# Kernel optimization log

Measured on AMD Instinct MI355X. Metric: run time of the kernel, lower is better.

## Reference

```python
import jax, jax.numpy as jnp
import numpy as np

EMBED_DIM = 256
NUM_HEADS = 8
TEMPERATURE = 10000.0
SCALE = 100.0
EPS = 1e-5


def setup_inputs() -> dict:
    key = jax.random.key(0)
    k1, k2, k3 = jax.random.split(key, 3)
    B, N, H, Wd = 1, 300, 24, 80
    # depths in a realistic positive range
    predict_depth = jax.random.uniform(k1, (B, N), dtype=jnp.float32) * 60.0
    depth_map = jax.random.uniform(k2, (B, H, Wd), dtype=jnp.float32) * 60.0
    # nn.Linear(embed_dim, num_heads): store as (in, out)
    W = jax.random.normal(k3, (EMBED_DIM, NUM_HEADS), dtype=jnp.float32) * 0.05
    b = jnp.zeros((NUM_HEADS,), dtype=jnp.float32)
    return {"predict_depth": predict_depth, "depth_map": depth_map, "W": W, "b": b}


def reference(predict_depth, depth_map, W, b):
    B, H, Wd = depth_map.shape
    HW = H * Wd
    N = predict_depth.shape[1]
    dm = depth_map.reshape(B, HW)
    pd = jax.nn.relu(predict_depth)
    # depth log-ratio: (B, N, HW)
    delta = jnp.log((pd[:, :, None] + EPS) / (dm[:, None, :] + EPS))
    # sine/cos embedding with interleaved sin/cos per frequency -> (B, N, HW, 256)
    dim_t = TEMPERATURE ** (jnp.arange(EMBED_DIM // 2, dtype=jnp.float32) * 2.0 / EMBED_DIM)
    pos = delta[..., None] * SCALE / dim_t  # (B, N, HW, 128)
    pos = jnp.stack((jnp.sin(pos), jnp.cos(pos)), axis=-1).reshape(B, N, HW, EMBED_DIM)
    # computed under torch.no_grad() in the original
    pos = jax.lax.stop_gradient(pos)
    # Linear(256 -> num_heads) + ReLU
    out = jax.nn.relu(pos @ W + b)  # (B, N, HW, heads)
    # permute(0,3,1,2).flatten(0,1) -> (B*heads, N, HW)
    out = jnp.transpose(out, (0, 3, 1, 2)).reshape(B * NUM_HEADS, N, HW)
    return out
```

## Files before the change

### kernel.cpp

```cpp
#include <hip/hip_runtime.h>
#include <hip/hip_bf16.h>

#define NPTS   300
#define HW_SZ  1920
#define TOTAL  (NPTS * HW_SZ)
#define NCOL   2400
#define L2T128 0.10381025293350249f

#define BM  64
#define BN  64
#define LDK 72
#define SNP 132
#define WTP 132
#define MT  30
#define CT  38

typedef __attribute__((ext_vector_type(8))) short short8;
typedef __attribute__((ext_vector_type(4))) float floatx4;

union frag_u { unsigned u[4]; short8 s; };

__device__ __forceinline__ unsigned pk_bf16(float lo, float hi) {
    return __builtin_amdgcn_perm(__float_as_uint(hi) + 0x8000u,
                                 __float_as_uint(lo) + 0x8000u,
                                 0x07060302u);
}

__global__ __launch_bounds__(256, 4) void dre_v10(const float* __restrict__ pd,
                                                  const float* __restrict__ dm,
                                                  const float* __restrict__ W,
                                                  const float* __restrict__ b,
                                                  float* __restrict__ out)
{
    __shared__ float kfr[128];
    __shared__ float ldm[BM];
    __shared__ float snq[8 * SNP];
    __shared__ float cnq[8 * SNP];
    __shared__ float wst[8 * WTP];
    __shared__ float wct[8 * WTP];
    __shared__ unsigned short Bs[2][BN * LDK];

    const int tid = threadIdx.x;
    const int m0  = blockIdx.x * BM;
    const int c0  = blockIdx.y * BN;
    const int n0  = c0 >> 3;

    if (tid < 128)      kfr[tid] = 100.0f * exp2f(-(float)tid * L2T128);
    else if (tid < 192) ldm[tid - 128] = __logf(dm[m0 + tid - 128] + 1e-5f);
#pragma unroll
    for (int v = 0; v < 8; ++v) {
        const int lin = tid * 8 + v;
        const int arr = lin >> 10, rest = lin & 1023;
        const int h = rest >> 7, i = rest & 127;
        const float val = W[i * 16 + arr * 8 + h];
        (arr ? wct : wst)[h * WTP + i] = val;
    }
    {
        const int nl = tid >> 5;
        const int nn = n0 + nl;
        const float pv = (nn < NPTS) ? pd[nn] : 0.0f;
        const float lp = __logf(fmaxf(pv, 0.0f) + 1e-5f);
#pragma unroll
        for (int j = 0; j < 4; ++j) {
            const int i = (tid & 31) * 4 + j;
            const float k = 100.0f * exp2f(-(float)i * L2T128);
            float s, c;
            __sincosf(k * lp, &s, &c);
            snq[nl * SNP + i] = s;
            cnq[nl * SNP + i] = c;
        }
    }

    const int w = tid >> 6, lane = tid & 63, quad = lane >> 4, l16 = lane & 15;
    const int bcr = tid >> 2, q = tid & 3;
    const int bnl = bcr >> 3, bh = bcr & 7;

    floatx4 acc[4];
#pragma unroll
    for (int nf = 0; nf < 4; ++nf) acc[nf] = (floatx4){0.f, 0.f, 0.f, 0.f};

    unsigned astash[2][2][4];
    unsigned qstash[2][8];

    __syncthreads();
    const float ld_row = ldm[w * 16 + l16];

#pragma unroll
    for (int ch = 0; ch < 4; ++ch) {
        const int ibase = (ch & 1) * 64;
        unsigned short* bsb = Bs[ch & 1];
        frag_u af[2];

        if (ch < 2) {
            unsigned pp[8];
#pragma unroll
            for (int g = 0; g < 4; ++g) {
                const int i4 = ibase + q * 16 + g * 4;
                const float4 s4 = *(const float4*)&snq[bnl * SNP + i4];
                const float4 c4 = *(const float4*)&cnq[bnl * SNP + i4];
                const float4 a4 = *(const float4*)&wst[bh * WTP + i4];
                const float4 o4 = *(const float4*)&wct[bh * WTP + i4];
                const float P0 = a4.x*s4.x + o4.x*c4.x, P1 = a4.y*s4.y + o4.y*c4.y;
                const float P2 = a4.z*s4.z + o4.z*c4.z, P3 = a4.w*s4.w + o4.w*c4.w;
                const float Q0 = o4.x*s4.x - a4.x*c4.x, Q1 = o4.y*s4.y - a4.y*c4.y;
                const float Q2 = o4.z*s4.z - a4.z*c4.z, Q3 = o4.w*s4.w - a4.w*c4.w;
                pp[2*g]   = pk_bf16(P0, P1);
                pp[2*g+1] = pk_bf16(P2, P3);
                qstash[ch][2*g]   = pk_bf16(Q0, Q1);
                qstash[ch][2*g+1] = pk_bf16(Q2, Q3);
            }
            *(uint4*)&bsb[bcr * LDK + q * 16]     = make_uint4(pp[0], pp[1], pp[2], pp[3]);
            *(uint4*)&bsb[bcr * LDK + q * 16 + 8] = make_uint4(pp[4], pp[5], pp[6], pp[7]);

#pragma unroll
            for (int ks = 0; ks < 2; ++ks) {
                const int kb = ibase + ks * 32 + quad * 8;
                const float4 f0 = *(const float4*)&kfr[kb];
                const float4 f1 = *(const float4*)&kfr[kb + 4];
                float s[8], c[8];
                __sincosf(f0.x * ld_row, &s[0], &c[0]);
                __sincosf(f0.y * ld_row, &s[1], &c[1]);
                __sincosf(f0.z * ld_row, &s[2], &c[2]);
                __sincosf(f0.w * ld_row, &s[3], &c[3]);
                __sincosf(f1.x * ld_row, &s[4], &c[4]);
                __sincosf(f1.y * ld_row, &s[5], &c[5]);
                __sincosf(f1.z * ld_row, &s[6], &c[6]);
                __sincosf(f1.w * ld_row, &s[7], &c[7]);
#pragma unroll
                for (int r = 0; r < 4; ++r) {
                    af[ks].u[r]          = pk_bf16(c[2*r], c[2*r+1]);
                    astash[ch][ks][r]    = pk_bf16(s[2*r], s[2*r+1]);
                }
            }
        } else {
            const unsigned* qs = qstash[ch - 2];
            *(uint4*)&bsb[bcr * LDK + q * 16]     = make_uint4(qs[0], qs[1], qs[2], qs[3]);
            *(uint4*)&bsb[bcr * LDK + q * 16 + 8] = make_uint4(qs[4], qs[5], qs[6], qs[7]);
#pragma unroll
            for (int ks = 0; ks < 2; ++ks)
#pragma unroll
                for (int r = 0; r < 4; ++r) af[ks].u[r] = astash[ch - 2][ks][r];
        }

        __syncthreads();

#pragma unroll
        for (int ks = 0; ks < 2; ++ks) {
            const int koff = ks * 32 + quad * 8;
#pragma unroll
            for (int nf = 0; nf < 4; ++nf) {
                short8 bb = *(const short8*)&bsb[(nf * 16 + l16) * LDK + koff];
                acc[nf] = __builtin_amdgcn_mfma_f32_16x16x32_bf16(af[ks].s, bb, acc[nf], 0, 0, 0);
            }
        }
    }

    const float bias = b[lane & 7];
#pragma unroll
    for (int nf = 0; nf < 4; ++nf) {
        const int c = c0 + nf * 16 + l16;
        if (c < NCOL) {
            const int n = c >> 3, h = c & 7;
            const int hw = m0 + w * 16 + quad * 4;
            floatx4 v = acc[nf];
            v.x = fmaxf(v.x + bias, 0.0f);
            v.y = fmaxf(v.y + bias, 0.0f);
            v.z = fmaxf(v.z + bias, 0.0f);
            v.w = fmaxf(v.w + bias, 0.0f);
            *(floatx4*)(out + (size_t)h * TOTAL + (size_t)n * HW_SZ + hw) = v;
        }
    }
}

extern "C" void kernel_launch(void* const* d_in, const int* in_sizes, int n_in,
                              void* d_out, int out_size, void* d_ws, size_t ws_size,
                              hipStream_t stream) {
    const float* pd = (const float*)d_in[0];
    const float* dm = (const float*)d_in[1];
    const float* W  = (const float*)d_in[2];
    const float* b  = (const float*)d_in[3];
    float* out = (float*)d_out;

    dre_v10<<<dim3(MT, CT), 256, 0, stream>>>(pd, dm, W, b, out);
}
```

Baseline: 78.08 us.

## Build full P/Q B-tiles upfront and drop per-chunk barriers and register stashes

Replaces the four-chunk double-buffered loop, which had a barrier per chunk and kept Q values and sine fragments in registers, with one prologue that writes complete P and Q bf16 tiles for all 128 frequencies into shared memory. After that a single barrier-free MFMA loop computes the sin/cos A fragments and issues paired MFMAs against the P and Q tiles. W is also stored packed as bf16 pairs in LDS, which halves weight LDS traffic but rounds W to bf16 before the P/Q products. The goal is fewer barriers and lower register pressure, at the cost of a larger shared-memory footprint and a serialized prologue that no longer overlaps with the MFMAs.

```diff
diff --git a/kernel.cpp b/kernel.cpp
--- a/kernel.cpp
+++ b/kernel.cpp
@@ -7,13 +7,13 @@
 #define NCOL   2400
 #define L2T128 0.10381025293350249f
 
-#define BM  64
-#define BN  64
-#define LDK 72
-#define SNP 132
-#define WTP 132
-#define MT  30
-#define CT  38
+#define BM   64
+#define BN   64
+#define LDK2 136
+#define SNP  132
+#define WPP  132
+#define MT   30
+#define CT   38
 
 typedef __attribute__((ext_vector_type(8))) short short8;
 typedef __attribute__((ext_vector_type(4))) float floatx4;
@@ -25,20 +25,22 @@
                                  __float_as_uint(lo) + 0x8000u,
                                  0x07060302u);
 }
+__device__ __forceinline__ float blo(unsigned u) { return __uint_as_float(u << 16); }
+__device__ __forceinline__ float bhi(unsigned u) { return __uint_as_float(u & 0xffff0000u); }
 
-__global__ __launch_bounds__(256, 4) void dre_v10(const float* __restrict__ pd,
+__global__ __launch_bounds__(256, 4) void dre_v11(const float* __restrict__ pd,
                                                   const float* __restrict__ dm,
                                                   const float* __restrict__ W,
                                                   const float* __restrict__ b,
                                                   float* __restrict__ out)
 {
-    __shared__ float kfr[128];
-    __shared__ float ldm[BM];
-    __shared__ float snq[8 * SNP];
-    __shared__ float cnq[8 * SNP];
-    __shared__ float wst[8 * WTP];
-    __shared__ float wct[8 * WTP];
-    __shared__ unsigned short Bs[2][BN * LDK];
+    __shared__ float    kfr[128];
+    __shared__ float    ldm[BM];
+    __shared__ float    snq[8 * SNP];
+    __shared__ float    cnq[8 * SNP];
+    __shared__ unsigned wpk[8 * WPP];
+    __shared__ unsigned short BsP[BN * LDK2];
+    __shared__ unsigned short BsQ[BN * LDK2];
 
     const int tid = threadIdx.x;
     const int m0  = blockIdx.x * BM;
@@ -47,110 +49,101 @@
 
     if (tid < 128)      kfr[tid] = 100.0f * exp2f(-(float)tid * L2T128);
     else if (tid < 192) ldm[tid - 128] = __logf(dm[m0 + tid - 128] + 1e-5f);
+    {
+        const int h = tid & 7, i0 = (tid >> 3) * 4;
+        unsigned pk[4];
 #pragma unroll
-    for (int v = 0; v < 8; ++v) {
-        const int lin = tid * 8 + v;
-        const int arr = lin >> 10, rest = lin & 1023;
-        const int h = rest >> 7, i = rest & 127;
-        const float val = W[i * 16 + arr * 8 + h];
-        (arr ? wct : wst)[h * WTP + i] = val;
+        for (int j = 0; j < 4; ++j)
+            pk[j] = pk_bf16(W[(i0 + j) * 16 + h], W[(i0 + j) * 16 + 8 + h]);
+        *(uint4*)&wpk[h * WPP + i0] = make_uint4(pk[0], pk[1], pk[2], pk[3]);
     }
     {
-        const int nl = tid >> 5;
+        const int nl = tid >> 5, i0 = (tid & 31) * 4;
         const int nn = n0 + nl;
         const float pv = (nn < NPTS) ? pd[nn] : 0.0f;
         const float lp = __logf(fmaxf(pv, 0.0f) + 1e-5f);
+        float s[4], c[4];
 #pragma unroll
         for (int j = 0; j < 4; ++j) {
-            const int i = (tid & 31) * 4 + j;
-            const float k = 100.0f * exp2f(-(float)i * L2T128);
-            float s, c;
-            __sincosf(k * lp, &s, &c);
-            snq[nl * SNP + i] = s;
-            cnq[nl * SNP + i] = c;
+            const float k = 100.0f * exp2f(-(float)(i0 + j) * L2T128);
+            __sincosf(k * lp, &s[j], &c[j]);
+        }
+        *(float4*)&snq[nl * SNP + i0] = make_float4(s[0], s[1], s[2], s[3]);
+        *(float4*)&cnq[nl * SNP + i0] = make_float4(c[0], c[1], c[2], c[3]);
+    }
+    __syncthreads();
+
+    {
+        const int bcr = tid >> 2, q = tid & 3;
+        const int bnl = bcr >> 3, bh = bcr & 7;
+#pragma unroll
+        for (int half = 0; half < 2; ++half) {
+            const int ib0 = q * 32 + half * 16;
+            unsigned pp[8], qq[8];
+#pragma unroll
+            for (int g = 0; g < 4; ++g) {
+                const int i4 = ib0 + g * 4;
+                const float4 s4 = *(const float4*)&snq[bnl * SNP + i4];
+                const float4 c4 = *(const float4*)&cnq[bnl * SNP + i4];
+                const uint4  w4 = *(const uint4*)&wpk[bh * WPP + i4];
+                const float ws0 = blo(w4.x), wc0 = bhi(w4.x);
+                const float ws1 = blo(w4.y), wc1 = bhi(w4.y);
+                const float ws2 = blo(w4.z), wc2 = bhi(w4.z);
+                const float ws3 = blo(w4.w), wc3 = bhi(w4.w);
+                const float P0 = ws0*s4.x + wc0*c4.x, Q0 = wc0*s4.x - ws0*c4.x;
+                const float P1 = ws1*s4.y + wc1*c4.y, Q1 = wc1*s4.y - ws1*c4.y;
+                const float P2 = ws2*s4.z + wc2*c4.z, Q2 = wc2*s4.z - ws2*c4.z;
+                const float P3 = ws3*s4.w + wc3*c4.w, Q3 = wc3*s4.w - ws3*c4.w;
+                pp[2*g] = pk_bf16(P0, P1);  pp[2*g+1] = pk_bf16(P2, P3);
+                qq[2*g] = pk_bf16(Q0, Q1);  qq[2*g+1] = pk_bf16(Q2, Q3);
+            }
+            *(uint4*)&BsP[bcr * LDK2 + ib0]     = make_uint4(pp[0], pp[1], pp[2], pp[3]);
+            *(uint4*)&BsP[bcr * LDK2 + ib0 + 8] = make_uint4(pp[4], pp[5], pp[6], pp[7]);
+            *(uint4*)&BsQ[bcr * LDK2 + ib0]     = make_uint4(qq[0], qq[1], qq[2], qq[3]);
+            *(uint4*)&BsQ[bcr * LDK2 + ib0 + 8] = make_uint4(qq[4], qq[5], qq[6], qq[7]);
         }
     }
+    __syncthreads();
 
     const int w = tid >> 6, lane = tid & 63, quad = lane >> 4, l16 = lane & 15;
-    const int bcr = tid >> 2, q = tid & 3;
-    const int bnl = bcr >> 3, bh = bcr & 7;
+    const float ld_row = ldm[w * 16 + l16];
 
     floatx4 acc[4];
 #pragma unroll
     for (int nf = 0; nf < 4; ++nf) acc[nf] = (floatx4){0.f, 0.f, 0.f, 0.f};
 
-    unsigned astash[2][2][4];
-    unsigned qstash[2][8];
-
-    __syncthreads();
-    const float ld_row = ldm[w * 16 + l16];
-
 #pragma unroll
-    for (int ch = 0; ch < 4; ++ch) {
-        const int ibase = (ch & 1) * 64;
-        unsigned short* bsb = Bs[ch & 1];
-        frag_u af[2];
-
-        if (ch < 2) {
-            unsigned pp[8];
-#pragma unroll
-            for (int g = 0; g < 4; ++g) {
-                const int i4 = ibase + q * 16 + g * 4;
-                const float4 s4 = *(const float4*)&snq[bnl * SNP + i4];
-                const float4 c4 = *(const float4*)&cnq[bnl * SNP + i4];
-                const float4 a4 = *(const float4*)&wst[bh * WTP + i4];
-                const float4 o4 = *(const float4*)&wct[bh * WTP + i4];
-                const float P0 = a4.x*s4.x + o4.x*c4.x, P1 = a4.y*s4.y + o4.y*c4.y;
-                const float P2 = a4.z*s4.z + o4.z*c4.z, P3 = a4.w*s4.w + o4.w*c4.w;
-                const float Q0 = o4.x*s4.x - a4.x*c4.x, Q1 = o4.y*s4.y - a4.y*c4.y;
-                const float Q2 = o4.z*s4.z - a4.z*c4.z, Q3 = o4.w*s4.w - a4.w*c4.w;
-                pp[2*g]   = pk_bf16(P0, P1);
-                pp[2*g+1] = pk_bf16(P2, P3);
-                qstash[ch][2*g]   = pk_bf16(Q0, Q1);
-                qstash[ch][2*g+1] = pk_bf16(Q2, Q3);
-            }
-            *(uint4*)&bsb[bcr * LDK + q * 16]     = make_uint4(pp[0], pp[1], pp[2], pp[3]);
-            *(uint4*)&bsb[bcr * LDK + q * 16 + 8] = make_uint4(pp[4], pp[5], pp[6], pp[7]);
-
-#pragma unroll
-            for (int ks = 0; ks < 2; ++ks) {
-                const int kb = ibase + ks * 32 + quad * 8;
-                const float4 f0 = *(const float4*)&kfr[kb];
-                const float4 f1 = *(const float4*)&kfr[kb + 4];
-                float s[8], c[8];
-                __sincosf(f0.x * ld_row, &s[0], &c[0]);
-                __sincosf(f0.y * ld_row, &s[1], &c[1]);
-                __sincosf(f0.z * ld_row, &s[2], &c[2]);
-                __sincosf(f0.w * ld_row, &s[3], &c[3]);
-                __sincosf(f1.x * ld_row, &s[4], &c[4]);
-                __sincosf(f1.y * ld_row, &s[5], &c[5]);
-                __sincosf(f1.z * ld_row, &s[6], &c[6]);
-                __sincosf(f1.w * ld_row, &s[7], &c[7]);
-#pragma unroll
-                for (int r = 0; r < 4; ++r) {
-                    af[ks].u[r]          = pk_bf16(c[2*r], c[2*r+1]);
-                    astash[ch][ks][r]    = pk_bf16(s[2*r], s[2*r+1]);
-                }
-            }
-        } else {
-            const unsigned* qs = qstash[ch - 2];
-            *(uint4*)&bsb[bcr * LDK + q * 16]     = make_uint4(qs[0], qs[1], qs[2], qs[3]);
-            *(uint4*)&bsb[bcr * LDK + q * 16 + 8] = make_uint4(qs[4], qs[5], qs[6], qs[7]);
-#pragma unroll
-            for (int ks = 0; ks < 2; ++ks)
-#pragma unroll
-                for (int r = 0; r < 4; ++r) af[ks].u[r] = astash[ch - 2][ks][r];
-        }
-
-        __syncthreads();
-
+    for (int ib = 0; ib < 2; ++ib) {
+        frag_u cf[2], sf[2];
 #pragma unroll
         for (int ks = 0; ks < 2; ++ks) {
-            const int koff = ks * 32 + quad * 8;
+            const int kb = ib * 64 + ks * 32 + quad * 8;
+            const float4 f0 = *(const float4*)&kfr[kb];
+            const float4 f1 = *(const float4*)&kfr[kb + 4];
+            float s[8], c[8];
+            __sincosf(f0.x * ld_row, &s[0], &c[0]);
+            __sincosf(f0.y * ld_row, &s[1], &c[1]);
+            __sincosf(f0.z * ld_row, &s[2], &c[2]);
+            __sincosf(f0.w * ld_row, &s[3], &c[3]);
+            __sincosf(f1.x * ld_row, &s[4], &c[4]);
+            __sincosf(f1.y * ld_row, &s[5], &c[5]);
+            __sincosf(f1.z * ld_row, &s[6], &c[6]);
+            __sincosf(f1.w * ld_row, &s[7], &c[7]);
+#pragma unroll
+            for (int r = 0; r < 4; ++r) {
+                cf[ks].u[r] = pk_bf16(c[2*r], c[2*r+1]);
+                sf[ks].u[r] = pk_bf16(s[2*r], s[2*r+1]);
+            }
+        }
+#pragma unroll
+        for (int ks = 0; ks < 2; ++ks) {
+            const int koff = ib * 64 + ks * 32 + quad * 8;
 #pragma unroll
             for (int nf = 0; nf < 4; ++nf) {
-                short8 bb = *(const short8*)&bsb[(nf * 16 + l16) * LDK + koff];
-                acc[nf] = __builtin_amdgcn_mfma_f32_16x16x32_bf16(af[ks].s, bb, acc[nf], 0, 0, 0);
+                short8 bp = *(const short8*)&BsP[(nf * 16 + l16) * LDK2 + koff];
+                acc[nf] = __builtin_amdgcn_mfma_f32_16x16x32_bf16(cf[ks].s, bp, acc[nf], 0, 0, 0);
+                short8 bq = *(const short8*)&BsQ[(nf * 16 + l16) * LDK2 + koff];
+                acc[nf] = __builtin_amdgcn_mfma_f32_16x16x32_bf16(sf[ks].s, bq, acc[nf], 0, 0, 0);
             }
         }
     }
@@ -181,5 +174,5 @@
     const float* b  = (const float*)d_in[3];
     float* out = (float*)d_out;
 
-    dre_v10<<<dim3(MT, CT), 256, 0, stream>>>(pd, dm, W, b, out);
+    dre_v11<<<dim3(MT, CT), 256, 0, stream>>>(pd, dm, W, b, out);
 }
```

Measured after the change: 74.50 us. 1.05x faster.
